# Optimization experiments

Hardware: AMD Instinct MI355X
Metric: run time of the kernel (lower is better)

Reference implementation:

```python
import jax, jax.numpy as jnp
import numpy as np

EPS = 1e-6

B, R, S, CSEM = 4, 16384, 48, 4


def setup_inputs() -> dict:
    key = jax.random.key(0)
    k1, k2, k3, k4, k5 = jax.random.split(key, 5)
    colors = jax.random.uniform(k1, (B, R, S, 3), dtype=jnp.float32)
    densities = jax.random.normal(k2, (B, R, S, 1), dtype=jnp.float32)
    # depths must be monotonically increasing along the sample axis
    depths = jnp.sort(jax.random.uniform(k3, (B, R, S, 1), dtype=jnp.float32) * 5.0 + 0.5, axis=2)
    # semantics: per-sample class probabilities in [0,1]
    semantics = jax.nn.softmax(jax.random.normal(k4, (B, R, S, CSEM), dtype=jnp.float32), axis=-1)
    levels = jax.random.randint(k5, (B,), 0, 3, dtype=jnp.int32)
    return {"colors": colors, "densities": densities, "depths": depths,
            "semantics": semantics, "levels": levels}


def reference(colors, densities, depths, semantics, levels):
    dtype = colors.dtype
    # midpoints along the sample axis (dim 2)
    deltas = depths[:, :, 1:] - depths[:, :, :-1]            # [B,R,S-1,1]
    colors_mid = (colors[:, :, :-1] + colors[:, :, 1:]) * 0.5
    densities_mid = (densities[:, :, :-1] + densities[:, :, 1:]) * 0.5
    depths_mid = (depths[:, :, :-1] + depths[:, :, 1:]) * 0.5
    sem_mid = (semantics[:, :, :-1] + semantics[:, :, 1:]) * 0.5

    densities_mid = jax.nn.softplus(densities_mid).astype(dtype)  # activation_factory
    alpha = 1.0 - jnp.exp(-densities_mid * deltas)                # [B,R,S-1,1]

    # per-batch level masking (vectorized version of the python loop)
    lv = levels[:, None, None, None]                              # [B,1,1,1]
    sem0 = sem_mid[..., 0:1]
    sem3 = sem_mid[..., 3:4]
    factor = jnp.where(lv == 1, 1.0 - sem0,
             jnp.where(lv == 2, 1.0 - sem0 - sem3, 1.0))
    alpha = alpha * factor

    # level 1: zero ch0, renormalize ch1..3
    tail = sem_mid[..., 1:]
    sem_l1 = jnp.concatenate(
        [jnp.zeros_like(sem0), (tail + EPS) / (tail.sum(-1, keepdims=True) + EPS)], -1)
    # level 2: zero ch0 and ch3, renormalize ch1..2
    mid2 = sem_mid[..., 1:3]
    sem_l2 = jnp.concatenate(
        [jnp.zeros_like(sem0), (mid2 + EPS) / (mid2.sum(-1, keepdims=True) + EPS),
         jnp.zeros_like(sem3)], -1)
    sem_mid = jnp.where(lv == 1, sem_l1, jnp.where(lv == 2, sem_l2, sem_mid))

    # transmittance via exclusive cumprod along sample axis
    alpha_shifted = jnp.concatenate(
        [jnp.ones_like(alpha[:, :, :1]), 1.0 - alpha + 1e-10], axis=-2)
    weights = (alpha * jnp.cumprod(alpha_shifted, axis=-2)[:, :, :-1]).astype(dtype)

    composite_rgb = jnp.sum(weights * colors_mid, axis=-2)       # [B,R,3]
    composite_depth = jnp.sum(weights * depths_mid, axis=-2)     # [B,R,1]
    composite_semantics = jnp.sum(weights * sem_mid, axis=-2)    # [B,R,CSEM]

    composite_depth = jnp.where(jnp.isnan(composite_depth), jnp.inf, composite_depth).astype(dtype)
    composite_depth = jnp.clip(composite_depth, depths.min(), depths.max())
    return composite_rgb, composite_depth, composite_semantics, weights
```

## Files before the change

kernel.cpp:

```cpp
#include <hip/hip_runtime.h>
#include <math.h>

#define EPSF 1e-6f
#define NB 4
#define NR 16384
#define NS 48
#define NSEG 47
#define NRAYS (NB * NR)
#define KL 16
#define SPL 3
#define RPT 4
#define TPB 64
#define NTILES (NRAYS / RPT)
#define NBLK 2816

#define LC 0
#define LSM 576
#define LD 1344
#define LZ 1536
#define BUFSZ 1744
#define LW LC
#define LP LSM

typedef const __attribute__((address_space(1))) void as1_cvoid;
typedef __attribute__((address_space(3))) void as3_void;

__device__ __forceinline__ float softplus_f(float x) {
    return fmaxf(x, 0.0f) + __logf(1.0f + __expf(-fabsf(x)));
}

__device__ __forceinline__ void stage(const float* __restrict__ colors,
                                      const float* __restrict__ semantics,
                                      const float* __restrict__ densities,
                                      const float* __restrict__ depths,
                                      int tile, float* buf, int lane) {
    const int ray0 = tile * RPT;
    const float* c = colors + (size_t)ray0 * 144;
    __builtin_amdgcn_global_load_lds((as1_cvoid*)(c + lane * 4),
                                     (as3_void*)(buf + LC), 16, 0, 0);
    __builtin_amdgcn_global_load_lds((as1_cvoid*)(c + 256 + lane * 4),
                                     (as3_void*)(buf + LC + 256), 16, 0, 0);
    if (lane < 16)
        __builtin_amdgcn_global_load_lds((as1_cvoid*)(c + 512 + lane * 4),
                                         (as3_void*)(buf + LC + 512), 16, 0, 0);
    const float* s = semantics + (size_t)ray0 * 192;
#pragma unroll
    for (int i = 0; i < 3; ++i)
        __builtin_amdgcn_global_load_lds((as1_cvoid*)(s + i * 256 + lane * 4),
                                         (as3_void*)(buf + LSM + i * 256), 16, 0,
                                         0);
    if (lane < 48) {
        __builtin_amdgcn_global_load_lds(
            (as1_cvoid*)(densities + (size_t)ray0 * 48 + lane * 4),
            (as3_void*)(buf + LD), 16, 0, 0);
        __builtin_amdgcn_global_load_lds(
            (as1_cvoid*)(depths + (size_t)ray0 * 48 + lane * 4),
            (as3_void*)(buf + LZ), 16, 0, 0);
    }
}

__device__ __forceinline__ void do_tile(float* lds, int tile, int lv,
                                        float* __restrict__ out, float& gmn,
                                        float& gmx, int lane, int r, int t) {
    const int ray0 = tile * RPT;

    if (lane < 4) {
        gmn = fminf(gmn, lds[LZ + lane * 48]);
        gmx = fmaxf(gmx, lds[LZ + lane * 48 + 47]);
    }

    const int cb = LC + r * 144 + 9 * t;
    const float4* sp = (const float4*)(lds + LSM + r * 192);
    const int db = LD + r * 48 + 3 * t;
    const int zb = LZ + r * 48 + 3 * t;

    float pc0 = lds[cb + 0], pc1 = lds[cb + 1], pc2 = lds[cb + 2];
    float4 psm = sp[3 * t];
    float pdn = lds[db], pz = lds[zb];

    float T = 1.0f;
    float wl[SPL];
    float acc_r = 0.f, acc_g = 0.f, acc_b = 0.f, acc_d = 0.f;
    float acc_s0 = 0.f, acc_s1 = 0.f, acc_s2 = 0.f, acc_s3 = 0.f;

#pragma unroll
    for (int j = 0; j < SPL; ++j) {
        float c0 = lds[cb + 3 * (j + 1)];
        float c1 = lds[cb + 3 * (j + 1) + 1];
        float c2 = lds[cb + 3 * (j + 1) + 2];
        float4 sm4 = sp[3 * t + j + 1];
        float dn = lds[db + j + 1];
        float z = lds[zb + j + 1];

        wl[j] = 0.0f;
        if (j < 2 || t < 15) {
            float delta = z - pz;
            float cm0 = (pc0 + c0) * 0.5f;
            float cm1 = (pc1 + c1) * 0.5f;
            float cm2 = (pc2 + c2) * 0.5f;
            float dnm = (pdn + dn) * 0.5f;
            float zm = (pz + z) * 0.5f;
            float sm0 = (psm.x + sm4.x) * 0.5f;
            float sm1 = (psm.y + sm4.y) * 0.5f;
            float sm2 = (psm.z + sm4.z) * 0.5f;
            float sm3 = (psm.w + sm4.w) * 0.5f;

            float sp_ = softplus_f(dnm);
            float alpha = 1.0f - __expf(-sp_ * delta);

            float factor, o0, o1, o2, o3;
            if (lv == 1) {
                factor = 1.0f - sm0;
                float inv = 1.0f / (sm1 + sm2 + sm3 + EPSF);
                o0 = 0.0f;
                o1 = (sm1 + EPSF) * inv;
                o2 = (sm2 + EPSF) * inv;
                o3 = (sm3 + EPSF) * inv;
            } else if (lv == 2) {
                factor = 1.0f - sm0 - sm3;
                float inv = 1.0f / (sm1 + sm2 + EPSF);
                o0 = 0.0f;
                o1 = (sm1 + EPSF) * inv;
                o2 = (sm2 + EPSF) * inv;
                o3 = 0.0f;
            } else {
                factor = 1.0f;
                o0 = sm0; o1 = sm1; o2 = sm2; o3 = sm3;
            }

            alpha *= factor;
            float w = alpha * T;
            T *= (1.0f - alpha + 1e-10f);
            wl[j] = w;

            acc_r += w * cm0;
            acc_g += w * cm1;
            acc_b += w * cm2;
            acc_d += w * zm;
            acc_s0 += w * o0;
            acc_s1 += w * o1;
            acc_s2 += w * o2;
            acc_s3 += w * o3;
        }
        pc0 = c0; pc1 = c1; pc2 = c2;
        psm = sm4; pdn = dn; pz = z;
    }

    float p = T;
#pragma unroll
    for (int off = 1; off < KL; off <<= 1) {
        float u = __shfl_up(p, off, KL);
        if (t >= off) p *= u;
    }
    float Tstart = __shfl_up(p, 1, KL);
    if (t == 0) Tstart = 1.0f;

    acc_r *= Tstart; acc_g *= Tstart; acc_b *= Tstart; acc_d *= Tstart;
    acc_s0 *= Tstart; acc_s1 *= Tstart; acc_s2 *= Tstart; acc_s3 *= Tstart;

#pragma unroll
    for (int j = 0; j < SPL; ++j) {
        if (j < 2 || t < 15)
            lds[LW + r * NSEG + 3 * t + j] = wl[j] * Tstart;
    }

    {
        const int pb = LP + r * 144 + t * 9;
        lds[pb + 0] = acc_r;  lds[pb + 1] = acc_g;
        lds[pb + 2] = acc_b;  lds[pb + 3] = acc_d;
        lds[pb + 4] = acc_s0; lds[pb + 5] = acc_s1;
        lds[pb + 6] = acc_s2; lds[pb + 7] = acc_s3;
    }

    if (lane < 47) {
        const float4* src = (const float4*)(lds + LW);
        float4* dst = (float4*)(out + (size_t)NRAYS * 8 + (size_t)ray0 * NSEG);
        dst[lane] = src[lane];
    }

    if (lane < 32) {
        const int rr = lane >> 3, qq = lane & 7;
        const int qb = LP + rr * 144 + qq;
        float v = 0.0f;
#pragma unroll
        for (int k = 0; k < KL; ++k) v += lds[qb + 9 * k];

        const int oray = ray0 + rr;
        size_t oidx;
        if (qq < 3) {
            oidx = (size_t)oray * 3 + qq;
        } else if (qq == 3) {
            if (isnan(v)) v = INFINITY;
            oidx = (size_t)NRAYS * 3 + oray;
        } else {
            oidx = (size_t)NRAYS * 4 + (size_t)oray * 4 + (qq - 4);
        }
        out[oidx] = v;
    }
}

__global__ __launch_bounds__(TPB) void march_kernel(
    const float* __restrict__ colors, const float* __restrict__ densities,
    const float* __restrict__ depths, const float* __restrict__ semantics,
    const int* __restrict__ levels, float2* __restrict__ ws2,
    float* __restrict__ out) {
    __shared__ float lds[2 * BUFSZ];
    const int lane = threadIdx.x;
    const int r = lane >> 4;
    const int t = lane & 15;
    float gmn = INFINITY, gmx = -INFINITY;

    int tile = blockIdx.x;
    float* curb = lds;
    float* nxtb = lds + BUFSZ;

    stage(colors, semantics, densities, depths, tile, curb, lane);

    int tnext = tile + NBLK;
    stage(colors, semantics, densities, depths, tnext, nxtb, lane);
    asm volatile("" ::: "memory");
    asm volatile("s_waitcnt vmcnt(8)" ::: "memory");
    do_tile(curb, tile, levels[tile >> 12], out, gmn, gmx, lane, r, t);
    { float* tmp = curb; curb = nxtb; nxtb = tmp; }
    tile = tnext;

    for (tnext = tile + NBLK; tnext < NTILES; tnext += NBLK) {
        stage(colors, semantics, densities, depths, tnext, nxtb, lane);
        asm volatile("" ::: "memory");
        asm volatile("s_waitcnt vmcnt(10)" ::: "memory");
        do_tile(curb, tile, levels[tile >> 12], out, gmn, gmx, lane, r, t);
        { float* tmp = curb; curb = nxtb; nxtb = tmp; }
        tile = tnext;
    }

    asm volatile("s_waitcnt vmcnt(2)" ::: "memory");
    do_tile(curb, tile, levels[tile >> 12], out, gmn, gmx, lane, r, t);

    gmn = fminf(gmn, __shfl_xor(gmn, 1, 4));
    gmn = fminf(gmn, __shfl_xor(gmn, 2, 4));
    gmx = fmaxf(gmx, __shfl_xor(gmx, 1, 4));
    gmx = fmaxf(gmx, __shfl_xor(gmx, 2, 4));
    if (lane == 0) ws2[blockIdx.x] = make_float2(gmn, gmx);
}

__global__ __launch_bounds__(256) void clip_depth(const float2* __restrict__ ws2,
                                                  float* __restrict__ dout) {
    __shared__ float smn[4], smx[4];
    float mn = INFINITY, mx = -INFINITY;
#pragma unroll
    for (int k = 0; k < NBLK / 256; ++k) {
        float2 v = ws2[threadIdx.x + (k << 8)];
        mn = fminf(mn, v.x);
        mx = fmaxf(mx, v.y);
    }
#pragma unroll
    for (int off = 32; off > 0; off >>= 1) {
        mn = fminf(mn, __shfl_down(mn, off));
        mx = fmaxf(mx, __shfl_down(mx, off));
    }
    if ((threadIdx.x & 63) == 0) {
        smn[threadIdx.x >> 6] = mn;
        smx[threadIdx.x >> 6] = mx;
    }
    __syncthreads();
    mn = fminf(fminf(smn[0], smn[1]), fminf(smn[2], smn[3]));
    mx = fmaxf(fmaxf(smx[0], smx[1]), fmaxf(smx[2], smx[3]));

    float4* d4 = (float4*)dout;
    const int i = blockIdx.x * 256 + threadIdx.x;
    float4 v = d4[i];
    v.x = fminf(fmaxf(v.x, mn), mx);
    v.y = fminf(fmaxf(v.y, mn), mx);
    v.z = fminf(fmaxf(v.z, mn), mx);
    v.w = fminf(fmaxf(v.w, mn), mx);
    d4[i] = v;
}

extern "C" void kernel_launch(void* const* d_in, const int* in_sizes, int n_in,
                              void* d_out, int out_size, void* d_ws, size_t ws_size,
                              hipStream_t stream) {
    const float* colors = (const float*)d_in[0];
    const float* densities = (const float*)d_in[1];
    const float* depths = (const float*)d_in[2];
    const float* semantics = (const float*)d_in[3];
    const int* levels = (const int*)d_in[4];
    float* out = (float*)d_out;
    float2* ws2 = (float2*)d_ws;

    march_kernel<<<NBLK, TPB, 0, stream>>>(colors, densities, depths, semantics,
                                           levels, ws2, out);
    clip_depth<<<64, 256, 0, stream>>>(ws2, out + (size_t)NRAYS * 3);
}
```

Before: 30.73 us.

## Replace persistent double-buffered loop with one tile per wave, many blocks

Drops the persistent grid-stride loop with double-buffered global_load_lds prefetch. Each wave now stages and processes exactly one 4-ray tile, with two waves per block and enough blocks to cover all tiles. Latency hiding now comes from hardware occupancy across many resident waves instead of manual software pipelining. The per-block depth min/max now goes through LDS and a block barrier, and the final clip reduction has to read more partial results, which adds some tail work.

```diff
diff --git a/kernel.cpp b/kernel.cpp
--- a/kernel.cpp
+++ b/kernel.cpp
@@ -10,9 +10,10 @@
 #define KL 16
 #define SPL 3
 #define RPT 4
-#define TPB 64
+#define WPB 2
+#define TPB (64 * WPB)
 #define NTILES (NRAYS / RPT)
-#define NBLK 2816
+#define NBLK (NTILES / WPB)
 
 #define LC 0
 #define LSM 576
@@ -21,6 +22,8 @@
 #define BUFSZ 1744
 #define LW LC
 #define LP LSM
+#define LX (WPB * BUFSZ)
+#define LTOT (LX + 2 * WPB)
 
 typedef const __attribute__((address_space(1))) void as1_cvoid;
 typedef __attribute__((address_space(3))) void as3_void;
@@ -59,24 +62,46 @@
     }
 }
 
-__device__ __forceinline__ void do_tile(float* lds, int tile, int lv,
-                                        float* __restrict__ out, float& gmn,
-                                        float& gmx, int lane, int r, int t) {
+__global__ __launch_bounds__(TPB) void march_kernel(
+    const float* __restrict__ colors, const float* __restrict__ densities,
+    const float* __restrict__ depths, const float* __restrict__ semantics,
+    const int* __restrict__ levels, float2* __restrict__ ws2,
+    float* __restrict__ out) {
+    __shared__ float lds[LTOT];
+    const int wid = threadIdx.x >> 6;
+    const int lane = threadIdx.x & 63;
+    const int r = lane >> 4;
+    const int t = lane & 15;
+    float* buf = lds + wid * BUFSZ;
+    const int tile = blockIdx.x * WPB + wid;
     const int ray0 = tile * RPT;
-
-    if (lane < 4) {
-        gmn = fminf(gmn, lds[LZ + lane * 48]);
-        gmx = fmaxf(gmx, lds[LZ + lane * 48 + 47]);
+    const int lv = levels[ray0 >> 14];
+
+    stage(colors, semantics, densities, depths, tile, buf, lane);
+    asm volatile("s_waitcnt vmcnt(0)" ::: "memory");
+
+    {
+        float a = (lane < 4) ? buf[LZ + lane * 48] : INFINITY;
+        float b = (lane < 4) ? buf[LZ + lane * 48 + 47] : -INFINITY;
+#pragma unroll
+        for (int k = 1; k < 4; k <<= 1) {
+            a = fminf(a, __shfl_xor(a, k, 4));
+            b = fmaxf(b, __shfl_xor(b, k, 4));
+        }
+        if (lane == 0) {
+            lds[LX + wid * 2] = a;
+            lds[LX + wid * 2 + 1] = b;
+        }
     }
 
     const int cb = LC + r * 144 + 9 * t;
-    const float4* sp = (const float4*)(lds + LSM + r * 192);
+    const float4* sp = (const float4*)(buf + LSM + r * 192);
     const int db = LD + r * 48 + 3 * t;
     const int zb = LZ + r * 48 + 3 * t;
 
-    float pc0 = lds[cb + 0], pc1 = lds[cb + 1], pc2 = lds[cb + 2];
+    float pc0 = buf[cb + 0], pc1 = buf[cb + 1], pc2 = buf[cb + 2];
     float4 psm = sp[3 * t];
-    float pdn = lds[db], pz = lds[zb];
+    float pdn = buf[db], pz = buf[zb];
 
     float T = 1.0f;
     float wl[SPL];
@@ -85,12 +110,12 @@
 
 #pragma unroll
     for (int j = 0; j < SPL; ++j) {
-        float c0 = lds[cb + 3 * (j + 1)];
-        float c1 = lds[cb + 3 * (j + 1) + 1];
-        float c2 = lds[cb + 3 * (j + 1) + 2];
+        float c0 = buf[cb + 3 * (j + 1)];
+        float c1 = buf[cb + 3 * (j + 1) + 1];
+        float c2 = buf[cb + 3 * (j + 1) + 2];
         float4 sm4 = sp[3 * t + j + 1];
-        float dn = lds[db + j + 1];
-        float z = lds[zb + j + 1];
+        float dn = buf[db + j + 1];
+        float z = buf[zb + j + 1];
 
         wl[j] = 0.0f;
         if (j < 2 || t < 15) {
@@ -161,19 +186,19 @@
 #pragma unroll
     for (int j = 0; j < SPL; ++j) {
         if (j < 2 || t < 15)
-            lds[LW + r * NSEG + 3 * t + j] = wl[j] * Tstart;
+            buf[LW + r * NSEG + 3 * t + j] = wl[j] * Tstart;
     }
 
     {
         const int pb = LP + r * 144 + t * 9;
-        lds[pb + 0] = acc_r;  lds[pb + 1] = acc_g;
-        lds[pb + 2] = acc_b;  lds[pb + 3] = acc_d;
-        lds[pb + 4] = acc_s0; lds[pb + 5] = acc_s1;
-        lds[pb + 6] = acc_s2; lds[pb + 7] = acc_s3;
+        buf[pb + 0] = acc_r;  buf[pb + 1] = acc_g;
+        buf[pb + 2] = acc_b;  buf[pb + 3] = acc_d;
+        buf[pb + 4] = acc_s0; buf[pb + 5] = acc_s1;
+        buf[pb + 6] = acc_s2; buf[pb + 7] = acc_s3;
     }
 
     if (lane < 47) {
-        const float4* src = (const float4*)(lds + LW);
+        const float4* src = (const float4*)(buf + LW);
         float4* dst = (float4*)(out + (size_t)NRAYS * 8 + (size_t)ray0 * NSEG);
         dst[lane] = src[lane];
     }
@@ -183,7 +208,7 @@
         const int qb = LP + rr * 144 + qq;
         float v = 0.0f;
 #pragma unroll
-        for (int k = 0; k < KL; ++k) v += lds[qb + 9 * k];
+        for (int k = 0; k < KL; ++k) v += buf[qb + 9 * k];
 
         const int oray = ray0 + rr;
         size_t oidx;
@@ -197,50 +222,13 @@
         }
         out[oidx] = v;
     }
-}
-
-__global__ __launch_bounds__(TPB) void march_kernel(
-    const float* __restrict__ colors, const float* __restrict__ densities,
-    const float* __restrict__ depths, const float* __restrict__ semantics,
-    const int* __restrict__ levels, float2* __restrict__ ws2,
-    float* __restrict__ out) {
-    __shared__ float lds[2 * BUFSZ];
-    const int lane = threadIdx.x;
-    const int r = lane >> 4;
-    const int t = lane & 15;
-    float gmn = INFINITY, gmx = -INFINITY;
-
-    int tile = blockIdx.x;
-    float* curb = lds;
-    float* nxtb = lds + BUFSZ;
-
-    stage(colors, semantics, densities, depths, tile, curb, lane);
-
-    int tnext = tile + NBLK;
-    stage(colors, semantics, densities, depths, tnext, nxtb, lane);
-    asm volatile("" ::: "memory");
-    asm volatile("s_waitcnt vmcnt(8)" ::: "memory");
-    do_tile(curb, tile, levels[tile >> 12], out, gmn, gmx, lane, r, t);
-    { float* tmp = curb; curb = nxtb; nxtb = tmp; }
-    tile = tnext;
-
-    for (tnext = tile + NBLK; tnext < NTILES; tnext += NBLK) {
-        stage(colors, semantics, densities, depths, tnext, nxtb, lane);
-        asm volatile("" ::: "memory");
-        asm volatile("s_waitcnt vmcnt(10)" ::: "memory");
-        do_tile(curb, tile, levels[tile >> 12], out, gmn, gmx, lane, r, t);
-        { float* tmp = curb; curb = nxtb; nxtb = tmp; }
-        tile = tnext;
-    }
-
-    asm volatile("s_waitcnt vmcnt(2)" ::: "memory");
-    do_tile(curb, tile, levels[tile >> 12], out, gmn, gmx, lane, r, t);
-
-    gmn = fminf(gmn, __shfl_xor(gmn, 1, 4));
-    gmn = fminf(gmn, __shfl_xor(gmn, 2, 4));
-    gmx = fmaxf(gmx, __shfl_xor(gmx, 1, 4));
-    gmx = fmaxf(gmx, __shfl_xor(gmx, 2, 4));
-    if (lane == 0) ws2[blockIdx.x] = make_float2(gmn, gmx);
+
+    __syncthreads();
+    if (threadIdx.x == 0) {
+        float mn = fminf(lds[LX + 0], lds[LX + 2]);
+        float mx = fmaxf(lds[LX + 1], lds[LX + 3]);
+        ws2[blockIdx.x] = make_float2(mn, mx);
+    }
 }
 
 __global__ __launch_bounds__(256) void clip_depth(const float2* __restrict__ ws2,
```

Result: faster. 28.97 us (-5.7%).
